# Performance work log

Measured on AMD Instinct MI355X. Metric: run time of the kernel, lower is better.

The kernel has to match this reference:

```python
import jax, jax.numpy as jnp
import numpy as np

NUM_FIELDS = 32
EMBED = 64
ATTN = 64
BATCH = 2048

# all field pairs (i < j), NC2 = 496
_ROW, _COL = np.triu_indices(NUM_FIELDS, k=1)
ROW_IDX = jnp.asarray(_ROW, dtype=jnp.int32)
COL_IDX = jnp.asarray(_COL, dtype=jnp.int32)


def setup_inputs() -> dict:
    key = jax.random.key(0)
    k0, k1, k2 = jax.random.split(key, 3)
    inputs = jax.random.normal(k0, (BATCH, NUM_FIELDS, EMBED), dtype=jnp.float32)
    # Linear init ~ U(-1/sqrt(fan_in), 1/sqrt(fan_in)) style scale
    W1 = jax.random.normal(k1, (EMBED, ATTN), dtype=jnp.float32) / jnp.sqrt(float(EMBED))
    b1 = jnp.zeros((ATTN,), dtype=jnp.float32)
    w2 = jax.random.normal(k2, (ATTN, 1), dtype=jnp.float32) / jnp.sqrt(float(ATTN))
    b2 = jnp.zeros((1,), dtype=jnp.float32)
    return {"inputs": inputs, "W1": W1, "b1": b1, "w2": w2, "b2": b2}


def reference(inputs, W1, b1, w2, b2):
    # inner: (B, P, E) pairwise elementwise products of field embeddings
    inner = inputs[:, ROW_IDX, :] * inputs[:, COL_IDX, :]
    # tiny 2-layer MLP attention: (B, P, E) -> (B, P, A) -> (B, P, 1)
    h = jax.nn.relu(jnp.einsum('bpe,ea->bpa', inner, W1) + b1)
    logits = jnp.einsum('bpa,ao->bpo', h, w2) + b2          # (B, P, 1)
    attn_scores = jax.nn.softmax(logits, axis=1)            # softmax over pair dim
    # softmax-weighted sum over pairs -> (B, E), then (B, 1, E)
    outputs = jnp.sum(attn_scores * inner, axis=1)
    return outputs[:, None, :], attn_scores
```

## Files before the change

kernel.cpp:

```cpp
#include <hip/hip_runtime.h>
#include <math.h>

#define NF 32
#define NE 64
#define NA 64
#define NP 496

typedef __attribute__((ext_vector_type(8))) _Float16 f16x8;
typedef __attribute__((ext_vector_type(4))) _Float16 f16x4;
typedef __attribute__((ext_vector_type(4))) float    f32x4;

#define W1T_S 72
#define XT_S  40
#define WT_S  40

__global__ __launch_bounds__(256, 2) void afm_fwd(
    const float* __restrict__ x,
    const float* __restrict__ W1,
    const float* __restrict__ b1,
    const float* __restrict__ w2,
    const float* __restrict__ b2,
    float* __restrict__ out,
    float* __restrict__ attn,
    int B)
{
    const int tid   = threadIdx.x;
    const int lane  = tid & 63;
    const int wv    = tid >> 6;
    const int nlane = lane & 15;
    const int g     = lane >> 4;

    __shared__ __align__(16) _Float16 W1t[64][W1T_S];
    __shared__ __align__(16) _Float16 xh[4][8][NF][8];
    __shared__ __align__(16) _Float16 xT[4][NE][XT_S];
    __shared__ __align__(16) _Float16 Wt[4][NF][WT_S];
    __shared__ float s_l[4][NP];
    __shared__ unsigned short s_rc[512];

    {
        const int e = tid & 63, a0 = (tid >> 6) << 4;
        const float* wr = W1 + e * NA + a0;
        #pragma unroll
        for (int i = 0; i < 4; ++i) {
            const float4 v = *(const float4*)(wr + 4 * i);
            W1t[a0 + 4*i + 0][e] = (_Float16)v.x;
            W1t[a0 + 4*i + 1][e] = (_Float16)v.y;
            W1t[a0 + 4*i + 2][e] = (_Float16)v.z;
            W1t[a0 + 4*i + 3][e] = (_Float16)v.w;
        }
    }
    for (int p = tid; p < 512; p += 256) {
        const int pp = (p < NP) ? p : NP - 1;
        const float sq = sqrtf((float)(3969 - 8 * pp));
        int r = (int)((63.0f - sq) * 0.5f);
        int st = (r * (63 - r)) >> 1;
        if (pp < st) { --r; st = (r * (63 - r)) >> 1; }
        else { const int st2 = ((r + 1) * (62 - r)) >> 1; if (pp >= st2) { ++r; st = st2; } }
        const int c = pp - st + r + 1;
        s_rc[p] = (unsigned short)(r | (c << 8));
    }
    __syncthreads();

    const int b = blockIdx.x * 4 + wv;
    if (b >= B) return;

    const float* __restrict__ xb = x + (size_t)b * (NF * NE);
    {
        const int r = lane >> 1, eh = (lane & 1) << 5;
        #pragma unroll
        for (int i = 0; i < 8; ++i) {
            const int e0 = eh + 4 * i;
            const float4 v = *(const float4*)(xb + r * NE + e0);
            f16x4 hv = { (_Float16)v.x, (_Float16)v.y, (_Float16)v.z, (_Float16)v.w };
            *(f16x4*)&xh[wv][e0 >> 3][r][e0 & 7] = hv;
            xT[wv][e0 + 0][r] = hv[0];
            xT[wv][e0 + 1][r] = hv[1];
            xT[wv][e0 + 2][r] = hv[2];
            xT[wv][e0 + 3][r] = hv[3];
        }
    }

    f16x8 w1f[2][4];
    #pragma unroll
    for (int s = 0; s < 2; ++s)
        #pragma unroll
        for (int mt = 0; mt < 4; ++mt)
            w1f[s][mt] = *(const f16x8*)&W1t[mt * 16 + nlane][s * 32 + g * 8];

    f32x4 b1q[4], w2q[4];
    #pragma unroll
    for (int mt = 0; mt < 4; ++mt) {
        b1q[mt] = *(const f32x4*)(b1 + mt * 16 + g * 4);
        w2q[mt] = *(const f32x4*)(w2 + mt * 16 + g * 4);
    }
    const float bias2 = b2[0];

    for (int t = 0; t < 31; ++t) {
        const int p0 = t << 4;
        const unsigned short rc = s_rc[p0 + nlane];
        const int r = rc & 255, c = rc >> 8;

        f16x8 af[2];
        #pragma unroll
        for (int s = 0; s < 2; ++s) {
            const f16x8 xr8 = *(const f16x8*)&xh[wv][4 * s + g][r][0];
            const f16x8 xc8 = *(const f16x8*)&xh[wv][4 * s + g][c][0];
            af[s] = xr8 * xc8;
        }
        f32x4 acc[4];
        #pragma unroll
        for (int mt = 0; mt < 4; ++mt) acc[mt] = b1q[mt];
        #pragma unroll
        for (int s = 0; s < 2; ++s)
            #pragma unroll
            for (int mt = 0; mt < 4; ++mt)
                acc[mt] = __builtin_amdgcn_mfma_f32_16x16x32_f16(w1f[s][mt], af[s], acc[mt], 0, 0, 0);

        float logit = 0.0f;
        #pragma unroll
        for (int mt = 0; mt < 4; ++mt) {
            logit = fmaf(fmaxf(acc[mt][0], 0.0f), w2q[mt][0], logit);
            logit = fmaf(fmaxf(acc[mt][1], 0.0f), w2q[mt][1], logit);
            logit = fmaf(fmaxf(acc[mt][2], 0.0f), w2q[mt][2], logit);
            logit = fmaf(fmaxf(acc[mt][3], 0.0f), w2q[mt][3], logit);
        }
        logit += __shfl_xor(logit, 16);
        logit += __shfl_xor(logit, 32);
        if (lane < 16) s_l[wv][p0 + lane] = logit + bias2;
    }

    float lv[8];
    float mx = -1e30f;
    #pragma unroll
    for (int k = 0; k < 8; ++k) {
        const int p = (k << 6) + lane;
        lv[k] = (p < NP) ? s_l[wv][p] : -1e30f;
        mx = fmaxf(mx, lv[k]);
    }
    #pragma unroll
    for (int off = 1; off < 64; off <<= 1) mx = fmaxf(mx, __shfl_xor(mx, off));

    float ev[8], se = 0.0f;
    #pragma unroll
    for (int k = 0; k < 8; ++k) {
        const int p = (k << 6) + lane;
        ev[k] = (p < NP) ? __expf(lv[k] - mx) : 0.0f;
        se += ev[k];
    }
    #pragma unroll
    for (int off = 1; off < 64; off <<= 1) se += __shfl_xor(se, off);
    const float inv = 1.0f / se;

    #pragma unroll
    for (int i = 0; i < 5; ++i) {
        f16x4 z = { (_Float16)0.f, (_Float16)0.f, (_Float16)0.f, (_Float16)0.f };
        ((f16x4*)&Wt[wv][0][0])[lane + (i << 6)] = z;
    }
    float* __restrict__ attn_b = attn + (size_t)b * NP;
    #pragma unroll
    for (int k = 0; k < 8; ++k) {
        const int p = (k << 6) + lane;
        if (p < NP) {
            const float w = ev[k] * inv;
            attn_b[p] = w;
            const unsigned short rc = s_rc[p];
            const int r = rc & 255, c = rc >> 8;
            const _Float16 wh = (_Float16)w;
            Wt[wv][r][c] = wh;
            Wt[wv][c][r] = wh;
        }
    }

    f16x8 wa[2], xbf[4];
    #pragma unroll
    for (int mt = 0; mt < 2; ++mt)
        wa[mt] = *(const f16x8*)&Wt[wv][mt * 16 + nlane][g * 8];
    #pragma unroll
    for (int nt = 0; nt < 4; ++nt)
        xbf[nt] = *(const f16x8*)&xT[wv][nt * 16 + nlane][g * 8];

    f32x4 y[2][4];
    #pragma unroll
    for (int mt = 0; mt < 2; ++mt)
        #pragma unroll
        for (int nt = 0; nt < 4; ++nt) {
            y[mt][nt] = (f32x4)0.0f;
            y[mt][nt] = __builtin_amdgcn_mfma_f32_16x16x32_f16(wa[mt], xbf[nt], y[mt][nt], 0, 0, 0);
        }

    float po[4] = {0.f, 0.f, 0.f, 0.f};
    #pragma unroll
    for (int nt = 0; nt < 4; ++nt)
        #pragma unroll
        for (int mt = 0; mt < 2; ++mt) {
            const f16x4 xv = *(const f16x4*)&xT[wv][nt * 16 + nlane][mt * 16 + g * 4];
            po[nt] += (float)xv[0] * y[mt][nt][0];
            po[nt] += (float)xv[1] * y[mt][nt][1];
            po[nt] += (float)xv[2] * y[mt][nt][2];
            po[nt] += (float)xv[3] * y[mt][nt][3];
        }
    #pragma unroll
    for (int nt = 0; nt < 4; ++nt) {
        po[nt] += __shfl_xor(po[nt], 16);
        po[nt] += __shfl_xor(po[nt], 32);
    }
    if (lane < 16) {
        float* __restrict__ ob = out + (size_t)b * NE;
        #pragma unroll
        for (int nt = 0; nt < 4; ++nt) ob[nt * 16 + lane] = 0.5f * po[nt];
    }
}

extern "C" void kernel_launch(void* const* d_in, const int* in_sizes, int n_in,
                              void* d_out, int out_size, void* d_ws, size_t ws_size,
                              hipStream_t stream) {
    const float* x  = (const float*)d_in[0];
    const float* W1 = (const float*)d_in[1];
    const float* b1 = (const float*)d_in[2];
    const float* w2 = (const float*)d_in[3];
    const float* b2 = (const float*)d_in[4];

    const int B = in_sizes[0] / (NF * NE);
    float* out_p  = (float*)d_out;
    float* attn_p = (float*)d_out + (size_t)B * NE;

    afm_fwd<<<(B + 3) / 4, 256, 0, stream>>>(x, W1, b1, w2, b2, out_p, attn_p, B);
}
```

Measured before the change: 23.80 us.

## Split each sample across two wavefronts with block-level sync

Each block now handles 2 samples instead of 4, with two wavefronts cooperating per sample. They split the pair-tile loop, the softmax scatter and the output matmul columns, and block-wide barriers coordinate them. This doubles the grid and halves per-wave serial work to shorten latency. The launch bound rises to 4 blocks per CU. The trade-off is extra __syncthreads, redundant softmax reductions in both waves, duplicated W1 staging per block, and the 16/15 tile split is slightly imbalanced.

```diff
diff --git a/kernel.cpp b/kernel.cpp
--- a/kernel.cpp
+++ b/kernel.cpp
@@ -14,7 +14,7 @@
 #define XT_S  40
 #define WT_S  40
 
-__global__ __launch_bounds__(256, 2) void afm_fwd(
+__global__ __launch_bounds__(256, 4) void afm_fwd(
     const float* __restrict__ x,
     const float* __restrict__ W1,
     const float* __restrict__ b1,
@@ -27,14 +27,16 @@
     const int tid   = threadIdx.x;
     const int lane  = tid & 63;
     const int wv    = tid >> 6;
+    const int smp   = wv >> 1;
+    const int sub   = wv & 1;
     const int nlane = lane & 15;
     const int g     = lane >> 4;
 
     __shared__ __align__(16) _Float16 W1t[64][W1T_S];
-    __shared__ __align__(16) _Float16 xh[4][8][NF][8];
-    __shared__ __align__(16) _Float16 xT[4][NE][XT_S];
-    __shared__ __align__(16) _Float16 Wt[4][NF][WT_S];
-    __shared__ float s_l[4][NP];
+    __shared__ __align__(16) _Float16 xh[2][8][NF][8];
+    __shared__ __align__(16) _Float16 xT[2][NE][XT_S];
+    __shared__ __align__(16) _Float16 Wt[2][NF][WT_S];
+    __shared__ float s_l[2][NP];
     __shared__ unsigned short s_rc[512];
 
     {
@@ -59,26 +61,36 @@
         const int c = pp - st + r + 1;
         s_rc[p] = (unsigned short)(r | (c << 8));
     }
-    __syncthreads();
-
-    const int b = blockIdx.x * 4 + wv;
-    if (b >= B) return;
+
+    int b = blockIdx.x * 2 + smp;
+    if (b >= B) b = B - 1;
+
+    {
+        unsigned int* wz = (unsigned int*)&Wt[smp][0][0];
+        #pragma unroll
+        for (int i = 0; i < 5; ++i) {
+            const int idx = i * 64 + lane;
+            if (idx < 320) wz[sub * 320 + idx] = 0u;
+        }
+    }
 
     const float* __restrict__ xb = x + (size_t)b * (NF * NE);
     {
-        const int r = lane >> 1, eh = (lane & 1) << 5;
-        #pragma unroll
-        for (int i = 0; i < 8; ++i) {
-            const int e0 = eh + 4 * i;
-            const float4 v = *(const float4*)(xb + r * NE + e0);
+        const int r  = sub * 16 + (lane >> 2);
+        const int e0 = (lane & 3) << 4;
+        #pragma unroll
+        for (int i = 0; i < 4; ++i) {
+            const int e = e0 + 4 * i;
+            const float4 v = *(const float4*)(xb + r * NE + e);
             f16x4 hv = { (_Float16)v.x, (_Float16)v.y, (_Float16)v.z, (_Float16)v.w };
-            *(f16x4*)&xh[wv][e0 >> 3][r][e0 & 7] = hv;
-            xT[wv][e0 + 0][r] = hv[0];
-            xT[wv][e0 + 1][r] = hv[1];
-            xT[wv][e0 + 2][r] = hv[2];
-            xT[wv][e0 + 3][r] = hv[3];
-        }
-    }
+            *(f16x4*)&xh[smp][e >> 3][r][e & 7] = hv;
+            xT[smp][e + 0][r] = hv[0];
+            xT[smp][e + 1][r] = hv[1];
+            xT[smp][e + 2][r] = hv[2];
+            xT[smp][e + 3][r] = hv[3];
+        }
+    }
+    __syncthreads();
 
     f16x8 w1f[2][4];
     #pragma unroll
@@ -95,7 +107,9 @@
     }
     const float bias2 = b2[0];
 
-    for (int t = 0; t < 31; ++t) {
+    const int t_end = sub ? 31 : 16;
+    #pragma unroll 2
+    for (int t = sub * 16; t < t_end; ++t) {
         const int p0 = t << 4;
         const unsigned short rc = s_rc[p0 + nlane];
         const int r = rc & 255, c = rc >> 8;
@@ -103,8 +117,8 @@
         f16x8 af[2];
         #pragma unroll
         for (int s = 0; s < 2; ++s) {
-            const f16x8 xr8 = *(const f16x8*)&xh[wv][4 * s + g][r][0];
-            const f16x8 xc8 = *(const f16x8*)&xh[wv][4 * s + g][c][0];
+            const f16x8 xr8 = *(const f16x8*)&xh[smp][4 * s + g][r][0];
+            const f16x8 xc8 = *(const f16x8*)&xh[smp][4 * s + g][c][0];
             af[s] = xr8 * xc8;
         }
         f32x4 acc[4];
@@ -126,15 +140,15 @@
         }
         logit += __shfl_xor(logit, 16);
         logit += __shfl_xor(logit, 32);
-        if (lane < 16) s_l[wv][p0 + lane] = logit + bias2;
-    }
-
-    float lv[8];
-    float mx = -1e30f;
+        if (lane < 16) s_l[smp][p0 + lane] = logit + bias2;
+    }
+    __syncthreads();
+
+    float lv[8], mx = -1e30f;
     #pragma unroll
     for (int k = 0; k < 8; ++k) {
         const int p = (k << 6) + lane;
-        lv[k] = (p < NP) ? s_l[wv][p] : -1e30f;
+        lv[k] = (p < NP) ? s_l[smp][p] : -1e30f;
         mx = fmaxf(mx, lv[k]);
     }
     #pragma unroll
@@ -151,63 +165,62 @@
     for (int off = 1; off < 64; off <<= 1) se += __shfl_xor(se, off);
     const float inv = 1.0f / se;
 
-    #pragma unroll
-    for (int i = 0; i < 5; ++i) {
-        f16x4 z = { (_Float16)0.f, (_Float16)0.f, (_Float16)0.f, (_Float16)0.f };
-        ((f16x4*)&Wt[wv][0][0])[lane + (i << 6)] = z;
-    }
     float* __restrict__ attn_b = attn + (size_t)b * NP;
     #pragma unroll
-    for (int k = 0; k < 8; ++k) {
-        const int p = (k << 6) + lane;
+    for (int k = 0; k < 4; ++k) {
+        const int kk = (sub << 2) + k;
+        const int p = (kk << 6) + lane;
         if (p < NP) {
-            const float w = ev[k] * inv;
+            const float w = ev[kk] * inv;
             attn_b[p] = w;
             const unsigned short rc = s_rc[p];
             const int r = rc & 255, c = rc >> 8;
             const _Float16 wh = (_Float16)w;
-            Wt[wv][r][c] = wh;
-            Wt[wv][c][r] = wh;
-        }
-    }
-
-    f16x8 wa[2], xbf[4];
+            Wt[smp][r][c] = wh;
+            Wt[smp][c][r] = wh;
+        }
+    }
+    __syncthreads();
+
+    f16x8 wa[2], xbf[2];
     #pragma unroll
     for (int mt = 0; mt < 2; ++mt)
-        wa[mt] = *(const f16x8*)&Wt[wv][mt * 16 + nlane][g * 8];
-    #pragma unroll
-    for (int nt = 0; nt < 4; ++nt)
-        xbf[nt] = *(const f16x8*)&xT[wv][nt * 16 + nlane][g * 8];
-
-    f32x4 y[2][4];
+        wa[mt] = *(const f16x8*)&Wt[smp][mt * 16 + nlane][g * 8];
+    #pragma unroll
+    for (int j = 0; j < 2; ++j) {
+        const int nt = 2 * sub + j;
+        xbf[j] = *(const f16x8*)&xT[smp][nt * 16 + nlane][g * 8];
+    }
+
+    f32x4 y[2][2];
     #pragma unroll
     for (int mt = 0; mt < 2; ++mt)
         #pragma unroll
-        for (int nt = 0; nt < 4; ++nt) {
-            y[mt][nt] = (f32x4)0.0f;
-            y[mt][nt] = __builtin_amdgcn_mfma_f32_16x16x32_f16(wa[mt], xbf[nt], y[mt][nt], 0, 0, 0);
-        }
-
-    float po[4] = {0.f, 0.f, 0.f, 0.f};
-    #pragma unroll
-    for (int nt = 0; nt < 4; ++nt)
+        for (int j = 0; j < 2; ++j) {
+            y[mt][j] = (f32x4)0.0f;
+            y[mt][j] = __builtin_amdgcn_mfma_f32_16x16x32_f16(wa[mt], xbf[j], y[mt][j], 0, 0, 0);
+        }
+
+    float po[2] = {0.f, 0.f};
+    #pragma unroll
+    for (int j = 0; j < 2; ++j) {
+        const int nt = 2 * sub + j;
         #pragma unroll
         for (int mt = 0; mt < 2; ++mt) {
-            const f16x4 xv = *(const f16x4*)&xT[wv][nt * 16 + nlane][mt * 16 + g * 4];
-            po[nt] += (float)xv[0] * y[mt][nt][0];
-            po[nt] += (float)xv[1] * y[mt][nt][1];
-            po[nt] += (float)xv[2] * y[mt][nt][2];
-            po[nt] += (float)xv[3] * y[mt][nt][3];
-        }
-    #pragma unroll
-    for (int nt = 0; nt < 4; ++nt) {
-        po[nt] += __shfl_xor(po[nt], 16);
-        po[nt] += __shfl_xor(po[nt], 32);
+            const f16x4 xv = *(const f16x4*)&xT[smp][nt * 16 + nlane][mt * 16 + g * 4];
+            po[j] += (float)xv[0] * y[mt][j][0];
+            po[j] += (float)xv[1] * y[mt][j][1];
+            po[j] += (float)xv[2] * y[mt][j][2];
+            po[j] += (float)xv[3] * y[mt][j][3];
+        }
+        po[j] += __shfl_xor(po[j], 16);
+        po[j] += __shfl_xor(po[j], 32);
     }
     if (lane < 16) {
         float* __restrict__ ob = out + (size_t)b * NE;
         #pragma unroll
-        for (int nt = 0; nt < 4; ++nt) ob[nt * 16 + lane] = 0.5f * po[nt];
+        for (int j = 0; j < 2; ++j)
+            ob[(2 * sub + j) * 16 + lane] = 0.5f * po[j];
     }
 }
 
@@ -224,5 +237,5 @@
     float* out_p  = (float*)d_out;
     float* attn_p = (float*)d_out + (size_t)B * NE;
 
-    afm_fwd<<<(B + 3) / 4, 256, 0, stream>>>(x, W1, b1, w2, b2, out_p, attn_p, B);
+    afm_fwd<<<(B + 1) / 2, 256, 0, stream>>>(x, W1, b1, w2, b2, out_p, attn_p, B);
 }
```

New measurement: 23.38 us. No clear change (-1.8%).

## Fuse softmax-weighted pair sum into logit loop with online unnormalized accumulation

Applied to the files above, without the earlier changes.

The pair-to-lane mapping changes so each of 16 lanes walks a contiguous run of 31 pairs, with row and column advanced incrementally instead of read from a shared lookup table. The exp of each logit is accumulated into per-lane output sums during the MLP loop, replacing the later transpose-and-MFMA weighted sum and its xT/Wt shared buffers. This removes shared-memory traffic, one sync and the second matmul phase, and cuts LDS use. In exchange it drops max subtraction, so exp can overflow for large logits, and it adds a cross-lane shuffle reduction of 16 accumulators.

```diff
diff --git a/kernel.cpp b/kernel.cpp
--- a/kernel.cpp
+++ b/kernel.cpp
@@ -5,14 +5,11 @@
 #define NE 64
 #define NA 64
 #define NP 496
+#define W1T_S 72
 
 typedef __attribute__((ext_vector_type(8))) _Float16 f16x8;
 typedef __attribute__((ext_vector_type(4))) _Float16 f16x4;
 typedef __attribute__((ext_vector_type(4))) float    f32x4;
-
-#define W1T_S 72
-#define XT_S  40
-#define WT_S  40
 
 __global__ __launch_bounds__(256, 2) void afm_fwd(
     const float* __restrict__ x,
@@ -32,10 +29,7 @@
 
     __shared__ __align__(16) _Float16 W1t[64][W1T_S];
     __shared__ __align__(16) _Float16 xh[4][8][NF][8];
-    __shared__ __align__(16) _Float16 xT[4][NE][XT_S];
-    __shared__ __align__(16) _Float16 Wt[4][NF][WT_S];
-    __shared__ float s_l[4][NP];
-    __shared__ unsigned short s_rc[512];
+    __shared__ float s_w[4][NP];
 
     {
         const int e = tid & 63, a0 = (tid >> 6) << 4;
@@ -49,20 +43,9 @@
             W1t[a0 + 4*i + 3][e] = (_Float16)v.w;
         }
     }
-    for (int p = tid; p < 512; p += 256) {
-        const int pp = (p < NP) ? p : NP - 1;
-        const float sq = sqrtf((float)(3969 - 8 * pp));
-        int r = (int)((63.0f - sq) * 0.5f);
-        int st = (r * (63 - r)) >> 1;
-        if (pp < st) { --r; st = (r * (63 - r)) >> 1; }
-        else { const int st2 = ((r + 1) * (62 - r)) >> 1; if (pp >= st2) { ++r; st = st2; } }
-        const int c = pp - st + r + 1;
-        s_rc[p] = (unsigned short)(r | (c << 8));
-    }
-    __syncthreads();
 
-    const int b = blockIdx.x * 4 + wv;
-    if (b >= B) return;
+    int b = blockIdx.x * 4 + wv;
+    if (b >= B) b = B - 1;
 
     const float* __restrict__ xb = x + (size_t)b * (NF * NE);
     {
@@ -73,12 +56,9 @@
             const float4 v = *(const float4*)(xb + r * NE + e0);
             f16x4 hv = { (_Float16)v.x, (_Float16)v.y, (_Float16)v.z, (_Float16)v.w };
             *(f16x4*)&xh[wv][e0 >> 3][r][e0 & 7] = hv;
-            xT[wv][e0 + 0][r] = hv[0];
-            xT[wv][e0 + 1][r] = hv[1];
-            xT[wv][e0 + 2][r] = hv[2];
-            xT[wv][e0 + 3][r] = hv[3];
         }
     }
+    __syncthreads();
 
     f16x8 w1f[2][4];
     #pragma unroll
@@ -95,119 +75,98 @@
     }
     const float bias2 = b2[0];
 
+    int pr, pc;
+    {
+        const int p0 = 31 * nlane;
+        const float sq = sqrtf((float)(3969 - 8 * p0));
+        int r = (int)((63.0f - sq) * 0.5f);
+        int st = (r * (63 - r)) >> 1;
+        if (p0 < st) { --r; st = (r * (63 - r)) >> 1; }
+        else { const int st2 = ((r + 1) * (62 - r)) >> 1; if (p0 >= st2) { ++r; st = st2; } }
+        pr = r; pc = p0 - st + r + 1;
+    }
+
+    float oacc0[8] = {0,0,0,0,0,0,0,0};
+    float oacc1[8] = {0,0,0,0,0,0,0,0};
+    float sw = 0.0f;
+
+    #pragma unroll 4
     for (int t = 0; t < 31; ++t) {
-        const int p0 = t << 4;
-        const unsigned short rc = s_rc[p0 + nlane];
-        const int r = rc & 255, c = rc >> 8;
+        const f16x8 xr0 = *(const f16x8*)&xh[wv][g][pr][0];
+        const f16x8 xc0 = *(const f16x8*)&xh[wv][g][pc][0];
+        const f16x8 xr1 = *(const f16x8*)&xh[wv][4 + g][pr][0];
+        const f16x8 xc1 = *(const f16x8*)&xh[wv][4 + g][pc][0];
+        const f16x8 af0 = xr0 * xc0;
+        const f16x8 af1 = xr1 * xc1;
 
-        f16x8 af[2];
-        #pragma unroll
-        for (int s = 0; s < 2; ++s) {
-            const f16x8 xr8 = *(const f16x8*)&xh[wv][4 * s + g][r][0];
-            const f16x8 xc8 = *(const f16x8*)&xh[wv][4 * s + g][c][0];
-            af[s] = xr8 * xc8;
-        }
         f32x4 acc[4];
         #pragma unroll
         for (int mt = 0; mt < 4; ++mt) acc[mt] = b1q[mt];
+        __builtin_amdgcn_s_setprio(1);
         #pragma unroll
-        for (int s = 0; s < 2; ++s)
-            #pragma unroll
-            for (int mt = 0; mt < 4; ++mt)
-                acc[mt] = __builtin_amdgcn_mfma_f32_16x16x32_f16(w1f[s][mt], af[s], acc[mt], 0, 0, 0);
+        for (int mt = 0; mt < 4; ++mt)
+            acc[mt] = __builtin_amdgcn_mfma_f32_16x16x32_f16(w1f[0][mt], af0, acc[mt], 0, 0, 0);
+        #pragma unroll
+        for (int mt = 0; mt < 4; ++mt)
+            acc[mt] = __builtin_amdgcn_mfma_f32_16x16x32_f16(w1f[1][mt], af1, acc[mt], 0, 0, 0);
+        __builtin_amdgcn_s_setprio(0);
 
-        float logit = 0.0f;
+        float pl0 = 0.f, pl1 = 0.f, pl2 = 0.f, pl3 = 0.f;
         #pragma unroll
         for (int mt = 0; mt < 4; ++mt) {
-            logit = fmaf(fmaxf(acc[mt][0], 0.0f), w2q[mt][0], logit);
-            logit = fmaf(fmaxf(acc[mt][1], 0.0f), w2q[mt][1], logit);
-            logit = fmaf(fmaxf(acc[mt][2], 0.0f), w2q[mt][2], logit);
-            logit = fmaf(fmaxf(acc[mt][3], 0.0f), w2q[mt][3], logit);
+            pl0 = fmaf(fmaxf(acc[mt][0], 0.f), w2q[mt][0], pl0);
+            pl1 = fmaf(fmaxf(acc[mt][1], 0.f), w2q[mt][1], pl1);
+            pl2 = fmaf(fmaxf(acc[mt][2], 0.f), w2q[mt][2], pl2);
+            pl3 = fmaf(fmaxf(acc[mt][3], 0.f), w2q[mt][3], pl3);
         }
+        float logit = (pl0 + pl1) + (pl2 + pl3);
         logit += __shfl_xor(logit, 16);
         logit += __shfl_xor(logit, 32);
-        if (lane < 16) s_l[wv][p0 + lane] = logit + bias2;
+
+        const float w = __expf(logit + bias2);
+        if (lane < 16) s_w[wv][31 * lane + t] = w;
+        sw += w;
+        #pragma unroll
+        for (int j = 0; j < 8; ++j) {
+            oacc0[j] = fmaf(w, (float)af0[j], oacc0[j]);
+            oacc1[j] = fmaf(w, (float)af1[j], oacc1[j]);
+        }
+
+        ++pc;
+        const int wrap = (pc >= 32) ? 1 : 0;
+        pr += wrap;
+        pc = wrap ? (pr + 1) : pc;
     }
 
-    float lv[8];
-    float mx = -1e30f;
     #pragma unroll
-    for (int k = 0; k < 8; ++k) {
-        const int p = (k << 6) + lane;
-        lv[k] = (p < NP) ? s_l[wv][p] : -1e30f;
-        mx = fmaxf(mx, lv[k]);
+    for (int off = 1; off < 16; off <<= 1) {
+        sw += __shfl_xor(sw, off);
+        #pragma unroll
+        for (int j = 0; j < 8; ++j) {
+            oacc0[j] += __shfl_xor(oacc0[j], off);
+            oacc1[j] += __shfl_xor(oacc1[j], off);
+        }
     }
-    #pragma unroll
-    for (int off = 1; off < 64; off <<= 1) mx = fmaxf(mx, __shfl_xor(mx, off));
+    const float inv = 1.0f / sw;
 
-    float ev[8], se = 0.0f;
-    #pragma unroll
-    for (int k = 0; k < 8; ++k) {
-        const int p = (k << 6) + lane;
-        ev[k] = (p < NP) ? __expf(lv[k] - mx) : 0.0f;
-        se += ev[k];
+    if (nlane == 0) {
+        float* __restrict__ ob = out + (size_t)b * NE;
+        f32x4 q;
+        q = (f32x4){oacc0[0]*inv, oacc0[1]*inv, oacc0[2]*inv, oacc0[3]*inv};
+        *(f32x4*)&ob[8*g + 0] = q;
+        q = (f32x4){oacc0[4]*inv, oacc0[5]*inv, oacc0[6]*inv, oacc0[7]*inv};
+        *(f32x4*)&ob[8*g + 4] = q;
+        q = (f32x4){oacc1[0]*inv, oacc1[1]*inv, oacc1[2]*inv, oacc1[3]*inv};
+        *(f32x4*)&ob[32 + 8*g + 0] = q;
+        q = (f32x4){oacc1[4]*inv, oacc1[5]*inv, oacc1[6]*inv, oacc1[7]*inv};
+        *(f32x4*)&ob[32 + 8*g + 4] = q;
     }
-    #pragma unroll
-    for (int off = 1; off < 64; off <<= 1) se += __shfl_xor(se, off);
-    const float inv = 1.0f / se;
 
-    #pragma unroll
-    for (int i = 0; i < 5; ++i) {
-        f16x4 z = { (_Float16)0.f, (_Float16)0.f, (_Float16)0.f, (_Float16)0.f };
-        ((f16x4*)&Wt[wv][0][0])[lane + (i << 6)] = z;
-    }
     float* __restrict__ attn_b = attn + (size_t)b * NP;
     #pragma unroll
     for (int k = 0; k < 8; ++k) {
         const int p = (k << 6) + lane;
-        if (p < NP) {
-            const float w = ev[k] * inv;
-            attn_b[p] = w;
-            const unsigned short rc = s_rc[p];
-            const int r = rc & 255, c = rc >> 8;
-            const _Float16 wh = (_Float16)w;
-            Wt[wv][r][c] = wh;
-            Wt[wv][c][r] = wh;
-        }
-    }
-
-    f16x8 wa[2], xbf[4];
-    #pragma unroll
-    for (int mt = 0; mt < 2; ++mt)
-        wa[mt] = *(const f16x8*)&Wt[wv][mt * 16 + nlane][g * 8];
-    #pragma unroll
-    for (int nt = 0; nt < 4; ++nt)
-        xbf[nt] = *(const f16x8*)&xT[wv][nt * 16 + nlane][g * 8];
-
-    f32x4 y[2][4];
-    #pragma unroll
-    for (int mt = 0; mt < 2; ++mt)
-        #pragma unroll
-        for (int nt = 0; nt < 4; ++nt) {
-            y[mt][nt] = (f32x4)0.0f;
-            y[mt][nt] = __builtin_amdgcn_mfma_f32_16x16x32_f16(wa[mt], xbf[nt], y[mt][nt], 0, 0, 0);
-        }
-
-    float po[4] = {0.f, 0.f, 0.f, 0.f};
-    #pragma unroll
-    for (int nt = 0; nt < 4; ++nt)
-        #pragma unroll
-        for (int mt = 0; mt < 2; ++mt) {
-            const f16x4 xv = *(const f16x4*)&xT[wv][nt * 16 + nlane][mt * 16 + g * 4];
-            po[nt] += (float)xv[0] * y[mt][nt][0];
-            po[nt] += (float)xv[1] * y[mt][nt][1];
-            po[nt] += (float)xv[2] * y[mt][nt][2];
-            po[nt] += (float)xv[3] * y[mt][nt][3];
-        }
-    #pragma unroll
-    for (int nt = 0; nt < 4; ++nt) {
-        po[nt] += __shfl_xor(po[nt], 16);
-        po[nt] += __shfl_xor(po[nt], 32);
-    }
-    if (lane < 16) {
-        float* __restrict__ ob = out + (size_t)b * NE;
-        #pragma unroll
-        for (int nt = 0; nt < 4; ++nt) ob[nt * 16 + lane] = 0.5f * po[nt];
+        if (p < NP) attn_b[p] = s_w[wv][p] * inv;
     }
 }
 
```

Result: slower. 45.25 us (+90.2%).
